# Kernel tuning notes

Hardware: AMD Instinct MI355X
Metric: run time of the kernel (lower is better)

## Reference

```python
import jax, jax.numpy as jnp
import numpy as np
from jax import lax

B = 2048      # batch
EMB = 128     # embedding_size
NF = 200      # num_filters
NR = 10000    # num_roles
NV = 50000    # num_values
ARITY = 5
EPS = 1e-5    # BatchNorm eps (torch default)


def setup_inputs() -> dict:
    key = jax.random.key(0)
    ks = jax.random.split(key, 12)
    bound = float(np.sqrt(1.0 / EMB))
    emb_roles = jax.random.uniform(ks[0], (NR, EMB), jnp.float32, -bound, bound).at[0].set(0.0)
    emb_values = jax.random.uniform(ks[1], (NV, EMB), jnp.float32, -bound, bound).at[0].set(0.0)
    D = NF * (EMB - 2)
    return {
        "x_batch": jax.random.randint(ks[2], (B, 2 * ARITY), 0, 10000),
        "arity": ARITY,
        "mode": 0,
        "emb_roles": emb_roles,
        "emb_values": emb_values,
        "conv1_w": jax.random.normal(ks[3], (NF, 1, 3, 3), jnp.float32) * 0.1,
        "conv1_b": jnp.zeros((NF,), jnp.float32),
        "bn1_gamma": jnp.ones((NF,), jnp.float32),
        "bn1_beta": jnp.zeros((NF,), jnp.float32),
        "conv2_w": jax.random.normal(ks[4], (NF, 1, 5, 3), jnp.float32) * 0.1,
        "conv2_b": jnp.zeros((NF,), jnp.float32),
        "bn2_gamma": jnp.ones((NF,), jnp.float32),
        "bn2_beta": jnp.zeros((NF,), jnp.float32),
        "fc_w": jax.random.normal(ks[5], (1, D), jnp.float32) * float(np.sqrt(2.0 / (D + 1))),
        "fc_b": jnp.zeros((1,), jnp.float32),
    }


def _conv(x, w, b):
    # x: [N,1,H,E], w: [F,1,kh,3] -> [N,F,1,E-2] (VALID conv; kh == H)
    y = lax.conv_general_dilated(x, w, (1, 1), 'VALID',
                                 dimension_numbers=('NCHW', 'OIHW', 'NCHW'))
    return y + b[None, :, None, None]


def reference(x_batch, arity, mode, emb_roles, emb_values,
              conv1_w, conv1_b, bn1_gamma, bn1_beta,
              conv2_w, conv2_b, bn2_gamma, bn2_beta, fc_w, fc_b):
    n = x_batch.shape[0]
    roles = x_batch[:, 0::2]
    vals = x_batch[:, 1::2]
    fr = emb_roles[roles[:, :2]]    # [B,2,E]
    fv = emb_values[vals[:, :2]]    # [B,2,E]
    # (head_value, role, tail_value) rows -> [B,3,E]
    hrt = jnp.stack([fv[:, 0], fr[:, 0], fv[:, 1]], axis=1)

    # primary triple branch: conv1 + BatchNorm (batch stats) + ReLU
    y1 = _conv(hrt[:, None], conv1_w, conv1_b)[:, :, 0, :]   # [B,F,E-2]
    m1 = y1.mean(axis=(0, 2), keepdims=True)
    v1 = y1.var(axis=(0, 2), keepdims=True)
    y1 = jax.nn.relu((y1 - m1) * jax.lax.rsqrt(v1 + EPS)
                     * bn1_gamma[None, :, None] + bn1_beta[None, :, None])
    feats = y1.reshape(n, -1)[:, None, :]                    # [B,1,D]

    if arity > 2:
        k = arity - 2
        kr = emb_roles[roles[:, 2:]]   # [B,K,E]
        kv = emb_values[vals[:, 2:]]   # [B,K,E]
        e = hrt.shape[-1]
        hrt_b = jnp.broadcast_to(hrt[:, None], (n, k, 3, e))
        x2 = jnp.concatenate([hrt_b, kr[:, :, None, :], kv[:, :, None, :]], axis=2)  # [B,K,5,E]
        y2 = _conv(x2.reshape(n * k, 1, 5, e), conv2_w, conv2_b)[:, :, 0, :]
        y2 = y2.reshape(n, k, y2.shape[1], y2.shape[2])      # [B,K,F,E-2]
        # original loop batch-norms each kv slot independently -> stats over (batch, width) per slot
        m2 = y2.mean(axis=(0, 3), keepdims=True)
        v2 = y2.var(axis=(0, 3), keepdims=True)
        y2 = jax.nn.relu((y2 - m2) * jax.lax.rsqrt(v2 + EPS)
                         * bn2_gamma[None, None, :, None] + bn2_beta[None, None, :, None])
        feats = jnp.concatenate([feats, y2.reshape(n, k, -1)], axis=1)  # [B,arity-1,D]

    min_val = feats.min(axis=1)                              # [B,D]
    return min_val @ fc_w.T + fc_b                           # [B,1]
```

## Files before the change

kernel.cpp:

```cpp
#include <hip/hip_runtime.h>

#define BB 2048
#define EMB 128
#define NF 200
#define W_OUT 126
#define EPS 1e-5f

#define NCOPY 8
#define FCWQ_BYTE_OFF 32768
#define FCWQ_HALFS (50 * 2 * 64 * 4)
#define WS_NEED (FCWQ_BYTE_OFF + FCWQ_HALFS * 2)

#define SPBS 4
#define STATS_BLOCKS (BB / SPBS)
#define SPBM 2
#define MAIN_BLOCKS (BB / SPBM)

typedef _Float16 half8 __attribute__((ext_vector_type(8)));
typedef _Float16 half4v __attribute__((ext_vector_type(4)));
typedef float f32x4v __attribute__((ext_vector_type(4)));

__device__ __forceinline__ const float* rowptr(const int* __restrict__ xr, int r,
                                               const float* __restrict__ er,
                                               const float* __restrict__ ev) {
  if (r == 0) return ev + (size_t)xr[1] * EMB;
  if (r == 1) return er + (size_t)xr[0] * EMB;
  if (r == 2) return ev + (size_t)xr[3] * EMB;
  const int k = (r - 3) >> 1;
  return ((r - 3) & 1) ? ev + (size_t)xr[5 + 2 * k] * EMB
                       : er + (size_t)xr[4 + 2 * k] * EMB;
}

__global__ __launch_bounds__(256, 2) void stats_mfma(
    const int* __restrict__ xb, const float* __restrict__ er,
    const float* __restrict__ ev, float* __restrict__ gout, int ncop,
    const float* __restrict__ fcw, _Float16* __restrict__ fcwQh, int do_swz) {
  __shared__ _Float16 Bt[SPBS][40][136];
  __shared__ float Gred[SPBS][1024];
  const int tid = threadIdx.x;
  const int base = blockIdx.x * SPBS;

  if (do_swz && blockIdx.x < (FCWQ_HALFS + 255) / 256) {
    const int idx = blockIdx.x * 256 + tid;
    if (idx < FCWQ_HALFS) {
      const int mtile = idx >> 9;
      const int rem = idx & 511;
      const int jh = rem >> 8;
      const int rem2 = rem & 255;
      const int l = rem2 >> 2;
      const int j = rem2 & 3;
      const int f = mtile * 4 + (l >> 4);
      const int x = (jh * 4 + j) * 16 + (l & 15);
      fcwQh[idx] = (_Float16)((x < W_OUT) ? fcw[(size_t)f * W_OUT + x] : 0.f);
    }
  }

  for (int job = tid; job < SPBS * 136; job += 256) {
    const int s = job / 136, x = job % 136;
    if (x < W_OUT) {
      const int* xr = xb + (size_t)(base + s) * 10;
#pragma unroll
      for (int r = 0; r < 9; r++) {
        const float* hp = rowptr(xr, r, er, ev);
        Bt[s][3 * r + 0][x] = (_Float16)hp[x];
        Bt[s][3 * r + 1][x] = (_Float16)hp[x + 1];
        Bt[s][3 * r + 2][x] = (_Float16)hp[x + 2];
      }
      Bt[s][27][x] = (_Float16)1.0f;
#pragma unroll
      for (int k = 28; k < 40; k++) Bt[s][k][x] = (_Float16)0.f;
    } else {
#pragma unroll
      for (int k = 0; k < 40; k++) Bt[s][k][x] = (_Float16)0.f;
    }
  }
  __syncthreads();

  const int w = tid >> 6, l = tid & 63;
  const int tl = l & 15, kl = l >> 4;
  f32x4v a00 = {0.f, 0.f, 0.f, 0.f}, a01 = a00, a10 = a00, a11 = a00;
#pragma unroll
  for (int c = 0; c < 4; c++) {
    const int x0 = c * 32 + kl * 8;
    const half8 g0 = *(const half8*)&Bt[w][tl][x0];
    const half8 g1 = *(const half8*)&Bt[w][16 + tl][x0];
    a00 = __builtin_amdgcn_mfma_f32_16x16x32_f16(g0, g0, a00, 0, 0, 0);
    a01 = __builtin_amdgcn_mfma_f32_16x16x32_f16(g0, g1, a01, 0, 0, 0);
    a10 = __builtin_amdgcn_mfma_f32_16x16x32_f16(g1, g0, a10, 0, 0, 0);
    a11 = __builtin_amdgcn_mfma_f32_16x16x32_f16(g1, g1, a11, 0, 0, 0);
  }
#pragma unroll
  for (int r = 0; r < 4; r++) {
    const int rm = kl * 4 + r;
    Gred[w][rm * 32 + tl]             = a00[r];
    Gred[w][rm * 32 + 16 + tl]        = a01[r];
    Gred[w][(16 + rm) * 32 + tl]      = a10[r];
    Gred[w][(16 + rm) * 32 + 16 + tl] = a11[r];
  }
  __syncthreads();
  float* gslice = gout + (blockIdx.x & (ncop - 1)) * 1024;
  for (int idx = tid; idx < 1024; idx += 256) {
    float s = Gred[0][idx] + Gred[1][idx] + Gred[2][idx] + Gred[3][idx];
    atomicAdd(&gslice[idx], s);
  }
}

template <bool SWZ>
__global__ __launch_bounds__(256, 2) void main_mfma(
    const int* __restrict__ xb, const float* __restrict__ er,
    const float* __restrict__ ev,
    const float* __restrict__ w1, const float* __restrict__ w2,
    const float* __restrict__ g1v, const float* __restrict__ be1,
    const float* __restrict__ g2v, const float* __restrict__ be2,
    const float* __restrict__ fcw, const _Float16* __restrict__ fcwQh,
    const float* __restrict__ fcb, const float* __restrict__ gbuf, int ncop,
    float* __restrict__ out) {
  __shared__ _Float16 AfL[50 * 64 * 8];
  __shared__ _Float16 Bm[SPBM][128][40];
  __shared__ float G[1024];
  __shared__ float red[4];
  const int tid = threadIdx.x;
  const int base = blockIdx.x * SPBM;

  for (int e = tid; e < 1024; e += 256) {
    float v = 0.f;
    for (int c = 0; c < ncop; c++) v += gbuf[c * 1024 + e];
    G[e] = v;
  }
  __syncthreads();

  {
    const int s = tid >> 7, x = tid & 127;
    const int* xr = xb + (size_t)(base + s) * 10;
    const int x1 = (x + 1 < 128) ? x + 1 : 127;
    const int x2 = (x + 2 < 128) ? x + 2 : 127;
    _Float16* dst = &Bm[s][x][0];
#pragma unroll
    for (int r = 0; r < 9; r++) {
      const float* hp = rowptr(xr, r, er, ev);
      dst[3 * r + 0] = (_Float16)hp[x];
      dst[3 * r + 1] = (_Float16)hp[x1];
      dst[3 * r + 2] = (_Float16)hp[x2];
    }
    dst[27] = (_Float16)1.0f;
#pragma unroll
    for (int k = 28; k < 40; k++) dst[k] = (_Float16)0.f;
  }

  const int f = tid;
  if (f < NF) {
    float w1r[9], w2r[15];
#pragma unroll
    for (int j = 0; j < 9; j++)  w1r[j] = w1[f * 9 + j];
#pragma unroll
    for (int j = 0; j < 15; j++) w2r[j] = w2[f * 15 + j];
    const float invN = 1.0f / (float)(BB * W_OUT);
    const int m = f >> 2, q4 = (f & 3) * 4;

    float m1 = 0.f, q1 = 0.f;
#pragma unroll
    for (int i = 0; i < 9; i++) {
      m1 = fmaf(w1r[i], G[i * 32 + 27], m1);
#pragma unroll
      for (int j = 0; j < 9; j++) q1 = fmaf(w1r[i] * w1r[j], G[i * 32 + j], q1);
    }
    m1 *= invN;
    float v1 = q1 * invN - m1 * m1;
    float sc1 = g1v[f] * rsqrtf(v1 + EPS);
    float sh1 = be1[f] - m1 * sc1;
    {
      float row[32];
#pragma unroll
      for (int k = 0; k < 32; k++) row[k] = 0.f;
#pragma unroll
      for (int i = 0; i < 9; i++) row[i] = w1r[i] * sc1;
      row[27] = sh1;
#pragma unroll
      for (int g = 0; g < 4; g++) {
        half8 h;
#pragma unroll
        for (int e = 0; e < 8; e++) h[e] = (_Float16)row[g * 8 + e];
        *(half8*)&AfL[(size_t)(m * 64 + g * 16 + q4 + 0) * 8] = h;
      }
    }

    float mcm = 0.f, qc = 0.f;
#pragma unroll
    for (int i = 0; i < 9; i++) {
      mcm = fmaf(w2r[i], G[i * 32 + 27], mcm);
#pragma unroll
      for (int j = 0; j < 9; j++) qc = fmaf(w2r[i] * w2r[j], G[i * 32 + j], qc);
    }
#pragma unroll
    for (int kk = 0; kk < 3; kk++) {
      const int a = 3 + 2 * kk, b = 4 + 2 * kk;
      float m2 = mcm, cross = 0.f, qa = 0.f, qb = 0.f, qab = 0.f;
#pragma unroll
      for (int j = 0; j < 3; j++) {
        m2 = fmaf(w2r[9 + j],  G[(3 * a + j) * 32 + 27], m2);
        m2 = fmaf(w2r[12 + j], G[(3 * b + j) * 32 + 27], m2);
      }
#pragma unroll
      for (int i = 0; i < 9; i++) {
        float t = 0.f;
#pragma unroll
        for (int j = 0; j < 3; j++) {
          t = fmaf(w2r[9 + j],  G[i * 32 + 3 * a + j], t);
          t = fmaf(w2r[12 + j], G[i * 32 + 3 * b + j], t);
        }
        cross = fmaf(w2r[i], t, cross);
      }
#pragma unroll
      for (int j = 0; j < 3; j++)
#pragma unroll
        for (int jp = 0; jp < 3; jp++) {
          qa  = fmaf(w2r[9 + j]  * w2r[9 + jp],  G[(3 * a + j) * 32 + 3 * a + jp], qa);
          qb  = fmaf(w2r[12 + j] * w2r[12 + jp], G[(3 * b + j) * 32 + 3 * b + jp], qb);
          qab = fmaf(w2r[9 + j]  * w2r[12 + jp], G[(3 * a + j) * 32 + 3 * b + jp], qab);
        }
      float q2 = qc + 2.f * cross + qa + qb + 2.f * qab;
      float mean2 = m2 * invN;
      float v2 = q2 * invN - mean2 * mean2;
      float sck = g2v[f] * rsqrtf(v2 + EPS);
      float shk = be2[f] - mean2 * sck;

      float row[32];
#pragma unroll
      for (int k = 0; k < 32; k++) row[k] = 0.f;
#pragma unroll
      for (int i = 0; i < 9; i++) row[i] = w2r[i] * sck;
#pragma unroll
      for (int j = 0; j < 3; j++) {
        row[3 * a + j] = w2r[9 + j]  * sck;
        row[3 * b + j] = w2r[12 + j] * sck;
      }
      row[27] = shk;
#pragma unroll
      for (int g = 0; g < 4; g++) {
        half8 h;
#pragma unroll
        for (int e = 0; e < 8; e++) h[e] = (_Float16)row[g * 8 + e];
        *(half8*)&AfL[(size_t)(m * 64 + g * 16 + q4 + 1 + kk) * 8] = h;
      }
    }
  }
  __syncthreads();

  const int w = tid >> 6, l = tid & 63;
  const int sW = w >> 1, mh = w & 1;
  const int xl = l & 15, fl = l >> 4;
  const float fcb0 = fcb[0];

  float psum = 0.f;
#pragma unroll 1
  for (int jh = 0; jh < 2; ++jh) {
    half8 bf[4];
#pragma unroll
    for (int j = 0; j < 4; ++j)
      bf[j] = *(const half8*)&Bm[sW][(jh * 4 + j) * 16 + xl][fl * 8];
#pragma unroll 1
    for (int mtb = 0; mtb < 5; ++mtb) {
      half8 af[5];
#pragma unroll
      for (int i = 0; i < 5; ++i) {
        const int mtile = mh * 25 + mtb * 5 + i;
        af[i] = *(const half8*)&AfL[(size_t)(mtile * 64 + l) * 8];
      }
#pragma unroll
      for (int i = 0; i < 5; ++i) {
        const int mtile = mh * 25 + mtb * 5 + i;
        const int fo = mtile * 4 + fl;
        half4v fqh;
        if (SWZ)
          fqh = *(const half4v*)&fcwQh[((size_t)(mtile * 2 + jh) * 64 + l) * 4];
#pragma unroll
        for (int j = 0; j < 4; ++j) {
          f32x4v acc = __builtin_amdgcn_mfma_f32_16x16x32_f16(
              af[i], bf[j], (f32x4v){0.f, 0.f, 0.f, 0.f}, 0, 0, 0);
          float fcv;
          if (SWZ) {
            fcv = (float)fqh[j];
          } else {
            const int x = (jh * 4 + j) * 16 + xl;
            const bool xv = (x < W_OUT);
            const float fcl = fcw[(size_t)fo * W_OUT + (xv ? x : 0)];
            fcv = xv ? fcl : 0.f;
          }
          float mv = fminf(fminf(fminf(acc[0], acc[1]), acc[2]), acc[3]);
          psum = fmaf(fmaxf(mv, 0.f), fcv, psum);
        }
      }
    }
  }

#pragma unroll
  for (int off = 32; off; off >>= 1) psum += __shfl_xor(psum, off, 64);
  if (l == 0) red[w] = psum;
  __syncthreads();
  if (tid < SPBM)
    out[base + tid] = red[2 * tid] + red[2 * tid + 1] + fcb0;
}

extern "C" void kernel_launch(void* const* d_in, const int* in_sizes, int n_in,
                              void* d_out, int out_size, void* d_ws, size_t ws_size,
                              hipStream_t stream) {
  const int* xb    = (const int*)d_in[0];
  const float* er  = (const float*)d_in[3];
  const float* ev  = (const float*)d_in[4];
  const float* w1  = (const float*)d_in[5];
  const float* g1  = (const float*)d_in[7];
  const float* be1 = (const float*)d_in[8];
  const float* w2  = (const float*)d_in[9];
  const float* g2  = (const float*)d_in[11];
  const float* be2 = (const float*)d_in[12];
  const float* fcw = (const float*)d_in[13];
  const float* fcb = (const float*)d_in[14];
  float* ws  = (float*)d_ws;
  float* out = (float*)d_out;

  const int full = (ws_size >= (size_t)WS_NEED) ? 1 : 0;
  float* gbuf = ws;
  _Float16* fcwQh = (_Float16*)((char*)d_ws + FCWQ_BYTE_OFF);
  const int ncop = full ? NCOPY : 1;

  hipMemsetAsync(gbuf, 0, (size_t)ncop * 1024 * sizeof(float), stream);
  hipLaunchKernelGGL(stats_mfma, dim3(STATS_BLOCKS), dim3(256), 0, stream,
                     xb, er, ev, gbuf, ncop, fcw, fcwQh, full);
  if (full)
    hipLaunchKernelGGL((main_mfma<true>), dim3(MAIN_BLOCKS), dim3(256), 0,
                       stream, xb, er, ev, w1, w2, g1, be1, g2, be2,
                       fcw, fcwQh, fcb, gbuf, ncop, out);
  else
    hipLaunchKernelGGL((main_mfma<false>), dim3(MAIN_BLOCKS), dim3(256), 0,
                       stream, xb, er, ev, w1, w2, g1, be1, g2, be2,
                       fcw, fcwQh, fcb, gbuf, ncop, out);
}
```

Measured before the change: 52.33 us.

## Hoist BN-folded weight computation into a single finalize kernel

Moves the per-filter batch-norm statistics solve and folded half-precision weight construction out of every main block into a one-block finalize kernel that writes the result to workspace. Main blocks now just copy the precomputed weight tile from global memory into LDS instead of reducing the Gram buffer and recomputing it. This removes redundant per-block arithmetic but adds a kernel launch and a serial single-block stage between stats and main.

```diff
diff --git a/kernel.cpp b/kernel.cpp
--- a/kernel.cpp
+++ b/kernel.cpp
@@ -9,7 +9,10 @@
 #define NCOPY 8
 #define FCWQ_BYTE_OFF 32768
 #define FCWQ_HALFS (50 * 2 * 64 * 4)
-#define WS_NEED (FCWQ_BYTE_OFF + FCWQ_HALFS * 2)
+#define AWF_BYTE_OFF 83968
+#define WS_NEED (AWF_BYTE_OFF + 50 * 64 * 8 * 2)
+#define AWF_FALLBACK_OFF 4096
+#define WS_FALLBACK_NEED (AWF_FALLBACK_OFF + 50 * 64 * 8 * 2)
 
 #define SPBS 4
 #define STATS_BLOCKS (BB / SPBS)
@@ -105,30 +108,135 @@
   }
 }
 
-template <bool SWZ>
-__global__ __launch_bounds__(256, 2) void main_mfma(
-    const int* __restrict__ xb, const float* __restrict__ er,
-    const float* __restrict__ ev,
+__global__ __launch_bounds__(256) void finalize_kernel(
     const float* __restrict__ w1, const float* __restrict__ w2,
-    const float* __restrict__ g1v, const float* __restrict__ be1,
-    const float* __restrict__ g2v, const float* __restrict__ be2,
-    const float* __restrict__ fcw, const _Float16* __restrict__ fcwQh,
-    const float* __restrict__ fcb, const float* __restrict__ gbuf, int ncop,
-    float* __restrict__ out) {
-  __shared__ _Float16 AfL[50 * 64 * 8];
-  __shared__ _Float16 Bm[SPBM][128][40];
+    const float* __restrict__ g1, const float* __restrict__ be1,
+    const float* __restrict__ g2, const float* __restrict__ be2,
+    const float* __restrict__ gbuf, _Float16* __restrict__ AwF, int ncop) {
   __shared__ float G[1024];
-  __shared__ float red[4];
   const int tid = threadIdx.x;
-  const int base = blockIdx.x * SPBM;
-
   for (int e = tid; e < 1024; e += 256) {
     float v = 0.f;
     for (int c = 0; c < ncop; c++) v += gbuf[c * 1024 + e];
     G[e] = v;
   }
   __syncthreads();
-
+  const int f = tid;
+  if (f >= NF) return;
+  float w1r[9], w2r[15];
+#pragma unroll
+  for (int j = 0; j < 9; j++)  w1r[j] = w1[f * 9 + j];
+#pragma unroll
+  for (int j = 0; j < 15; j++) w2r[j] = w2[f * 15 + j];
+  const float invN = 1.0f / (float)(BB * W_OUT);
+  const int m = f >> 2, q4 = (f & 3) * 4;
+
+  float m1 = 0.f, q1 = 0.f;
+#pragma unroll
+  for (int i = 0; i < 9; i++) {
+    m1 = fmaf(w1r[i], G[i * 32 + 27], m1);
+#pragma unroll
+    for (int j = 0; j < 9; j++) q1 = fmaf(w1r[i] * w1r[j], G[i * 32 + j], q1);
+  }
+  m1 *= invN;
+  float v1 = q1 * invN - m1 * m1;
+  float sc1 = g1[f] * rsqrtf(v1 + EPS);
+  float sh1 = be1[f] - m1 * sc1;
+  {
+    float row[32];
+#pragma unroll
+    for (int k = 0; k < 32; k++) row[k] = 0.f;
+#pragma unroll
+    for (int i = 0; i < 9; i++) row[i] = w1r[i] * sc1;
+    row[27] = sh1;
+#pragma unroll
+    for (int g = 0; g < 4; g++) {
+      half8 h;
+#pragma unroll
+      for (int e = 0; e < 8; e++) h[e] = (_Float16)row[g * 8 + e];
+      *(half8*)&AwF[(size_t)(m * 64 + g * 16 + q4 + 0) * 8] = h;
+    }
+  }
+
+  float mcm = 0.f, qc = 0.f;
+#pragma unroll
+  for (int i = 0; i < 9; i++) {
+    mcm = fmaf(w2r[i], G[i * 32 + 27], mcm);
+#pragma unroll
+    for (int j = 0; j < 9; j++) qc = fmaf(w2r[i] * w2r[j], G[i * 32 + j], qc);
+  }
+#pragma unroll
+  for (int kk = 0; kk < 3; kk++) {
+    const int a = 3 + 2 * kk, b = 4 + 2 * kk;
+    float m2 = mcm, cross = 0.f, qa = 0.f, qb = 0.f, qab = 0.f;
+#pragma unroll
+    for (int j = 0; j < 3; j++) {
+      m2 = fmaf(w2r[9 + j],  G[(3 * a + j) * 32 + 27], m2);
+      m2 = fmaf(w2r[12 + j], G[(3 * b + j) * 32 + 27], m2);
+    }
+#pragma unroll
+    for (int i = 0; i < 9; i++) {
+      float t = 0.f;
+#pragma unroll
+      for (int j = 0; j < 3; j++) {
+        t = fmaf(w2r[9 + j],  G[i * 32 + 3 * a + j], t);
+        t = fmaf(w2r[12 + j], G[i * 32 + 3 * b + j], t);
+      }
+      cross = fmaf(w2r[i], t, cross);
+    }
+#pragma unroll
+    for (int j = 0; j < 3; j++)
+#pragma unroll
+      for (int jp = 0; jp < 3; jp++) {
+        qa  = fmaf(w2r[9 + j]  * w2r[9 + jp],  G[(3 * a + j) * 32 + 3 * a + jp], qa);
+        qb  = fmaf(w2r[12 + j] * w2r[12 + jp], G[(3 * b + j) * 32 + 3 * b + jp], qb);
+        qab = fmaf(w2r[9 + j]  * w2r[12 + jp], G[(3 * a + j) * 32 + 3 * b + jp], qab);
+      }
+    float q2 = qc + 2.f * cross + qa + qb + 2.f * qab;
+    float mean2 = m2 * invN;
+    float v2 = q2 * invN - mean2 * mean2;
+    float sck = g2[f] * rsqrtf(v2 + EPS);
+    float shk = be2[f] - mean2 * sck;
+
+    float row[32];
+#pragma unroll
+    for (int k = 0; k < 32; k++) row[k] = 0.f;
+#pragma unroll
+    for (int i = 0; i < 9; i++) row[i] = w2r[i] * sck;
+#pragma unroll
+    for (int j = 0; j < 3; j++) {
+      row[3 * a + j] = w2r[9 + j]  * sck;
+      row[3 * b + j] = w2r[12 + j] * sck;
+    }
+    row[27] = shk;
+#pragma unroll
+    for (int g = 0; g < 4; g++) {
+      half8 h;
+#pragma unroll
+      for (int e = 0; e < 8; e++) h[e] = (_Float16)row[g * 8 + e];
+      *(half8*)&AwF[(size_t)(m * 64 + g * 16 + q4 + 1 + kk) * 8] = h;
+    }
+  }
+}
+
+template <bool SWZ>
+__global__ __launch_bounds__(256, 2) void main_mfma(
+    const int* __restrict__ xb, const float* __restrict__ er,
+    const float* __restrict__ ev, const float* __restrict__ fcw,
+    const _Float16* __restrict__ fcwQh, const _Float16* __restrict__ AwF,
+    const float* __restrict__ fcb, float* __restrict__ out) {
+  __shared__ _Float16 AfL[50 * 64 * 8];
+  __shared__ _Float16 Bm[SPBM][128][40];
+  __shared__ float red[4];
+  const int tid = threadIdx.x;
+  const int base = blockIdx.x * SPBM;
+
+  {
+    const uint2* __restrict__ Ag = (const uint2*)AwF;
+    uint2* Al = (uint2*)AfL;
+#pragma unroll
+    for (int i = 0; i < 25; ++i) Al[tid + i * 256] = Ag[tid + i * 256];
+  }
   {
     const int s = tid >> 7, x = tid & 127;
     const int* xr = xb + (size_t)(base + s) * 10;
@@ -145,104 +253,6 @@
     dst[27] = (_Float16)1.0f;
 #pragma unroll
     for (int k = 28; k < 40; k++) dst[k] = (_Float16)0.f;
-  }
-
-  const int f = tid;
-  if (f < NF) {
-    float w1r[9], w2r[15];
-#pragma unroll
-    for (int j = 0; j < 9; j++)  w1r[j] = w1[f * 9 + j];
-#pragma unroll
-    for (int j = 0; j < 15; j++) w2r[j] = w2[f * 15 + j];
-    const float invN = 1.0f / (float)(BB * W_OUT);
-    const int m = f >> 2, q4 = (f & 3) * 4;
-
-    float m1 = 0.f, q1 = 0.f;
-#pragma unroll
-    for (int i = 0; i < 9; i++) {
-      m1 = fmaf(w1r[i], G[i * 32 + 27], m1);
-#pragma unroll
-      for (int j = 0; j < 9; j++) q1 = fmaf(w1r[i] * w1r[j], G[i * 32 + j], q1);
-    }
-    m1 *= invN;
-    float v1 = q1 * invN - m1 * m1;
-    float sc1 = g1v[f] * rsqrtf(v1 + EPS);
-    float sh1 = be1[f] - m1 * sc1;
-    {
-      float row[32];
-#pragma unroll
-      for (int k = 0; k < 32; k++) row[k] = 0.f;
-#pragma unroll
-      for (int i = 0; i < 9; i++) row[i] = w1r[i] * sc1;
-      row[27] = sh1;
-#pragma unroll
-      for (int g = 0; g < 4; g++) {
-        half8 h;
-#pragma unroll
-        for (int e = 0; e < 8; e++) h[e] = (_Float16)row[g * 8 + e];
-        *(half8*)&AfL[(size_t)(m * 64 + g * 16 + q4 + 0) * 8] = h;
-      }
-    }
-
-    float mcm = 0.f, qc = 0.f;
-#pragma unroll
-    for (int i = 0; i < 9; i++) {
-      mcm = fmaf(w2r[i], G[i * 32 + 27], mcm);
-#pragma unroll
-      for (int j = 0; j < 9; j++) qc = fmaf(w2r[i] * w2r[j], G[i * 32 + j], qc);
-    }
-#pragma unroll
-    for (int kk = 0; kk < 3; kk++) {
-      const int a = 3 + 2 * kk, b = 4 + 2 * kk;
-      float m2 = mcm, cross = 0.f, qa = 0.f, qb = 0.f, qab = 0.f;
-#pragma unroll
-      for (int j = 0; j < 3; j++) {
-        m2 = fmaf(w2r[9 + j],  G[(3 * a + j) * 32 + 27], m2);
-        m2 = fmaf(w2r[12 + j], G[(3 * b + j) * 32 + 27], m2);
-      }
-#pragma unroll
-      for (int i = 0; i < 9; i++) {
-        float t = 0.f;
-#pragma unroll
-        for (int j = 0; j < 3; j++) {
-          t = fmaf(w2r[9 + j],  G[i * 32 + 3 * a + j], t);
-          t = fmaf(w2r[12 + j], G[i * 32 + 3 * b + j], t);
-        }
-        cross = fmaf(w2r[i], t, cross);
-      }
-#pragma unroll
-      for (int j = 0; j < 3; j++)
-#pragma unroll
-        for (int jp = 0; jp < 3; jp++) {
-          qa  = fmaf(w2r[9 + j]  * w2r[9 + jp],  G[(3 * a + j) * 32 + 3 * a + jp], qa);
-          qb  = fmaf(w2r[12 + j] * w2r[12 + jp], G[(3 * b + j) * 32 + 3 * b + jp], qb);
-          qab = fmaf(w2r[9 + j]  * w2r[12 + jp], G[(3 * a + j) * 32 + 3 * b + jp], qab);
-        }
-      float q2 = qc + 2.f * cross + qa + qb + 2.f * qab;
-      float mean2 = m2 * invN;
-      float v2 = q2 * invN - mean2 * mean2;
-      float sck = g2v[f] * rsqrtf(v2 + EPS);
-      float shk = be2[f] - mean2 * sck;
-
-      float row[32];
-#pragma unroll
-      for (int k = 0; k < 32; k++) row[k] = 0.f;
-#pragma unroll
-      for (int i = 0; i < 9; i++) row[i] = w2r[i] * sck;
-#pragma unroll
-      for (int j = 0; j < 3; j++) {
-        row[3 * a + j] = w2r[9 + j]  * sck;
-        row[3 * b + j] = w2r[12 + j] * sck;
-      }
-      row[27] = shk;
-#pragma unroll
-      for (int g = 0; g < 4; g++) {
-        half8 h;
-#pragma unroll
-        for (int e = 0; e < 8; e++) h[e] = (_Float16)row[g * 8 + e];
-        *(half8*)&AfL[(size_t)(m * 64 + g * 16 + q4 + 1 + kk) * 8] = h;
-      }
-    }
   }
   __syncthreads();
 
@@ -321,17 +331,19 @@
   const int full = (ws_size >= (size_t)WS_NEED) ? 1 : 0;
   float* gbuf = ws;
   _Float16* fcwQh = (_Float16*)((char*)d_ws + FCWQ_BYTE_OFF);
+  _Float16* AwF = (_Float16*)((char*)d_ws +
+                              (full ? AWF_BYTE_OFF : AWF_FALLBACK_OFF));
   const int ncop = full ? NCOPY : 1;
 
   hipMemsetAsync(gbuf, 0, (size_t)ncop * 1024 * sizeof(float), stream);
   hipLaunchKernelGGL(stats_mfma, dim3(STATS_BLOCKS), dim3(256), 0, stream,
                      xb, er, ev, gbuf, ncop, fcw, fcwQh, full);
+  hipLaunchKernelGGL(finalize_kernel, dim3(1), dim3(256), 0, stream,
+                     w1, w2, g1, be1, g2, be2, gbuf, AwF, ncop);
   if (full)
     hipLaunchKernelGGL((main_mfma<true>), dim3(MAIN_BLOCKS), dim3(256), 0,
-                       stream, xb, er, ev, w1, w2, g1, be1, g2, be2,
-                       fcw, fcwQh, fcb, gbuf, ncop, out);
+                       stream, xb, er, ev, fcw, fcwQh, AwF, fcb, out);
   else
     hipLaunchKernelGGL((main_mfma<false>), dim3(MAIN_BLOCKS), dim3(256), 0,
-                       stream, xb, er, ev, w1, w2, g1, be1, g2, be2,
-                       fcw, fcwQh, fcb, gbuf, ncop, out);
-}
+                       stream, xb, er, ev, fcw, fcwQh, AwF, fcb, out);
+}
```

Measured after the change: 47.42 us. 1.1x faster.
